# Optimization experiments

Measured on AMD Instinct MI355X. Metric: run time of the kernel, lower is better.

The kernel has to match this reference:

```python
import jax, jax.numpy as jnp
import numpy as np

BATCH, NUM_CENTERS, NUM_FEATURES = 8192, 2048, 512


def setup_inputs() -> dict:
    key = jax.random.key(0)
    k1, k2 = jax.random.split(key)
    inputs = jax.random.normal(k1, (BATCH, NUM_FEATURES), dtype=jnp.float32)
    centers = jax.random.normal(k2, (NUM_CENTERS, NUM_FEATURES), dtype=jnp.float32)
    sigmas = jnp.ones((NUM_CENTERS,), dtype=jnp.float32)
    return {"inputs": inputs, "centers": centers, "sigmas": sigmas}


def reference(inputs, centers, sigmas):
    # instead of materializing the [B, C, F] broadcast intermediate.
    x_sq = jnp.sum(inputs * inputs, axis=-1, keepdims=True)        # [B, 1]
    c_sq = jnp.sum(centers * centers, axis=-1)                     # [C]
    cross = jnp.einsum('bf,cf->bc', inputs, centers)               # [B, C]
    dists = x_sq + c_sq[None, :] - 2.0 * cross                     # [B, C]
    dists = jnp.maximum(dists, 0.0)  # guard tiny negatives from fp error
    return jnp.exp(-dists / (2.0 * sigmas * sigmas))               # [B, C]
```

## Files before the change

### kernel.cpp

```cpp
#include <hip/hip_runtime.h>
#include <hip/hip_bf16.h>
#include <stdint.h>


#define BATCH 8192
#define NCENT 2048
#define NFEAT 512

typedef float f32x4 __attribute__((ext_vector_type(4)));
typedef int   i32x8 __attribute__((ext_vector_type(8)));
typedef __bf16 bf16x8 __attribute__((ext_vector_type(8)));

union Frag8 {
    uint4 q[2];
    i32x8 v;
};
union FragAB {
    uint4 u;
    bf16x8 v;
};

static __device__ __forceinline__ unsigned int pack_bf16(float a, float b) {
    unsigned int ua = __builtin_bit_cast(unsigned int, a);
    unsigned int ub = __builtin_bit_cast(unsigned int, b);
    ua = (ua + 0x7fffu + ((ua >> 16) & 1u)) >> 16;
    ub = (ub + 0x7fffu + ((ub >> 16) & 1u)) >> 16;
    return ua | (ub << 16);
}

static __device__ __forceinline__ void llds16(const void* g, void* l) {
    __builtin_amdgcn_global_load_lds(
        (const __attribute__((address_space(1))) unsigned int*)g,
        (__attribute__((address_space(3))) unsigned int*)(uintptr_t)l,
        16, 0, 0);
}

__global__ __launch_bounds__(256) void convert_kernel(const float* __restrict__ X,
                                                      const float* __restrict__ Cn,
                                                      unsigned char* __restrict__ Xf8,
                                                      unsigned char* __restrict__ Cf8,
                                                      float* __restrict__ xsq,
                                                      float* __restrict__ csq) {
    const int bid  = blockIdx.x;
    const int lane = threadIdx.x & 63;
    const float* src;
    unsigned char* dst;
    float* nrm;
    int row;
    if (bid < BATCH / 4) {
        row = bid * 4 + (threadIdx.x >> 6);
        src = X; dst = Xf8; nrm = xsq;
    } else {
        row = (bid - BATCH / 4) * 4 + (threadIdx.x >> 6);
        src = Cn; dst = Cf8; nrm = csq;
    }
    const float4* p = (const float4*)(src + (size_t)row * NFEAT);
    float4 a = p[2 * lane];
    float4 b = p[2 * lane + 1];
    unsigned int lo = 0, hi = 0;
    lo = __builtin_amdgcn_cvt_pk_fp8_f32(a.x, a.y, lo, 0);
    lo = __builtin_amdgcn_cvt_pk_fp8_f32(a.z, a.w, lo, 1);
    hi = __builtin_amdgcn_cvt_pk_fp8_f32(b.x, b.y, hi, 0);
    hi = __builtin_amdgcn_cvt_pk_fp8_f32(b.z, b.w, hi, 1);
    ((uint2*)(dst + (size_t)row * NFEAT))[lane] = make_uint2(lo, hi);
    float s = a.x * a.x + a.y * a.y + a.z * a.z + a.w * a.w
            + b.x * b.x + b.y * b.y + b.z * b.z + b.w * b.w;
#pragma unroll
    for (int off = 32; off >= 1; off >>= 1) s += __shfl_down(s, off);
    if (lane == 0) nrm[row] = s;
}

__global__ __launch_bounds__(256) void rbf_gemm_fp8_kernel(
        const unsigned char* __restrict__ Xf8,
        const unsigned char* __restrict__ Cf8,
        const float* __restrict__ Sg,
        const float* __restrict__ xsq,
        const float* __restrict__ csq,
        float* __restrict__ out) {
    __shared__ unsigned char As[128 * 128];
    __shared__ unsigned char Bs[128 * 128];

    const int tid    = threadIdx.x;
    const int lane   = tid & 63;
    const int wave   = tid >> 6;
    const int wave_m = wave >> 1;
    const int wave_n = wave & 1;

    const int bid = blockIdx.x;
    const int xcd = bid & 7;
    const int j   = bid >> 3;
    const int bm0 = (xcd * 8 + (j >> 4)) * 128;
    const int bn0 = (j & 15) * 128;

    f32x4 acc[4][4];
#pragma unroll
    for (int i = 0; i < 4; ++i)
#pragma unroll
        for (int jj = 0; jj < 4; ++jj) acc[i][jj] = (f32x4){0.f, 0.f, 0.f, 0.f};

    const int fr   = lane & 15;
    const int quad = lane >> 4;

#pragma unroll
    for (int k0 = 0; k0 < NFEAT; k0 += 128) {
        __syncthreads();
#pragma unroll
        for (int i = 0; i < 4; ++i) {
            const int s   = (wave * 4 + i) * 64 + lane;
            const int row = s >> 3;
            const int c   = (s & 7) ^ (row & 7);
            llds16(Xf8 + (size_t)(bm0 + row) * NFEAT + k0 + c * 16,
                   As + (wave * 4 + i) * 1024);
            llds16(Cf8 + (size_t)(bn0 + row) * NFEAT + k0 + c * 16,
                   Bs + (wave * 4 + i) * 1024);
        }
        __syncthreads();

        Frag8 a[4], b[4];
#pragma unroll
        for (int mi = 0; mi < 4; ++mi) {
            const int row = wave_m * 64 + mi * 16 + fr;
            const unsigned char* base = As + row * 128;
            a[mi].q[0] = *(const uint4*)(base + ((quad * 2 + 0) ^ (row & 7)) * 16);
            a[mi].q[1] = *(const uint4*)(base + ((quad * 2 + 1) ^ (row & 7)) * 16);
        }
#pragma unroll
        for (int nj = 0; nj < 4; ++nj) {
            const int row = wave_n * 64 + nj * 16 + fr;
            const unsigned char* base = Bs + row * 128;
            b[nj].q[0] = *(const uint4*)(base + ((quad * 2 + 0) ^ (row & 7)) * 16);
            b[nj].q[1] = *(const uint4*)(base + ((quad * 2 + 1) ^ (row & 7)) * 16);
        }
#pragma unroll
        for (int mi = 0; mi < 4; ++mi)
#pragma unroll
            for (int nj = 0; nj < 4; ++nj)
                acc[mi][nj] = __builtin_amdgcn_mfma_scale_f32_16x16x128_f8f6f4(
                    a[mi].v, b[nj].v, acc[mi][nj],
                    0, 0,
                    0, 0x7F7F7F7F,
                    0, 0x7F7F7F7F);
    }

    const int col = lane & 15;
    const int rq  = lane >> 4;
#pragma unroll
    for (int nj = 0; nj < 4; ++nj) {
        const int n      = bn0 + wave_n * 64 + nj * 16 + col;
        const float csqn = csq[n];
        const float sg   = Sg[n];
        const float inv  = 0.5f / (sg * sg);
#pragma unroll
        for (int mi = 0; mi < 4; ++mi) {
            const int mbase = bm0 + wave_m * 64 + mi * 16 + rq * 4;
#pragma unroll
            for (int r = 0; r < 4; ++r) {
                const int m = mbase + r;
                float d = xsq[m] + csqn - 2.0f * acc[mi][nj][r];
                d = fmaxf(d, 0.0f);
                out[(size_t)m * NCENT + n] = __expf(-d * inv);
            }
        }
    }
}

__global__ __launch_bounds__(256) void sumsq_kernel(const float* __restrict__ src,
                                                    float* __restrict__ dst) {
    const int row  = blockIdx.x * 4 + (threadIdx.x >> 6);
    const int lane = threadIdx.x & 63;
    const float4* p = (const float4*)(src + (size_t)row * NFEAT);
    float4 a = p[lane];
    float4 b = p[lane + 64];
    float s = a.x * a.x + a.y * a.y + a.z * a.z + a.w * a.w
            + b.x * b.x + b.y * b.y + b.z * b.z + b.w * b.w;
#pragma unroll
    for (int off = 32; off >= 1; off >>= 1) s += __shfl_down(s, off);
    if (lane == 0) dst[row] = s;
}

__global__ __launch_bounds__(256) void rbf_fallback_kernel(const float* __restrict__ X,
                                                           const float* __restrict__ Cn,
                                                           const float* __restrict__ Sg,
                                                           const float* __restrict__ xsq,
                                                           const float* __restrict__ csq,
                                                           float* __restrict__ out) {
    __shared__ unsigned int As[128 * 16];
    __shared__ unsigned int Bs[128 * 16];

    const int tid    = threadIdx.x;
    const int lane   = tid & 63;
    const int wave   = tid >> 6;
    const int wave_m = wave >> 1;
    const int wave_n = wave & 1;
    const int bm0 = blockIdx.y * 128;
    const int bn0 = blockIdx.x * 128;

    f32x4 acc[4][4];
#pragma unroll
    for (int i = 0; i < 4; ++i)
#pragma unroll
        for (int j = 0; j < 4; ++j) acc[i][j] = (f32x4){0.f, 0.f, 0.f, 0.f};

    for (int k0 = 0; k0 < NFEAT; k0 += 32) {
        __syncthreads();
#pragma unroll
        for (int j = 0; j < 4; ++j) {
            const int s    = j * 256 + tid;
            const int row  = s >> 3;
            const int col4 = s & 7;
            {
                const float4 f = *(const float4*)(X + (size_t)(bm0 + row) * NFEAT + k0 + col4 * 4);
                *(uint2*)&As[row * 16 + col4 * 2] =
                    make_uint2(pack_bf16(f.x, f.y), pack_bf16(f.z, f.w));
            }
            {
                const float4 f = *(const float4*)(Cn + (size_t)(bn0 + row) * NFEAT + k0 + col4 * 4);
                *(uint2*)&Bs[row * 16 + col4 * 2] =
                    make_uint2(pack_bf16(f.x, f.y), pack_bf16(f.z, f.w));
            }
        }
        __syncthreads();

        const int fr   = lane & 15;
        const int quad = lane >> 4;
        FragAB a[4], b[4];
#pragma unroll
        for (int mi = 0; mi < 4; ++mi)
            a[mi].u = *(const uint4*)&As[(wave_m * 64 + mi * 16 + fr) * 16 + quad * 4];
#pragma unroll
        for (int nj = 0; nj < 4; ++nj)
            b[nj].u = *(const uint4*)&Bs[(wave_n * 64 + nj * 16 + fr) * 16 + quad * 4];
#pragma unroll
        for (int mi = 0; mi < 4; ++mi)
#pragma unroll
            for (int nj = 0; nj < 4; ++nj)
                acc[mi][nj] = __builtin_amdgcn_mfma_f32_16x16x32_bf16(
                    a[mi].v, b[nj].v, acc[mi][nj], 0, 0, 0);
    }

    const int col = lane & 15;
    const int rq  = lane >> 4;
#pragma unroll
    for (int nj = 0; nj < 4; ++nj) {
        const int n      = bn0 + wave_n * 64 + nj * 16 + col;
        const float csqn = csq[n];
        const float sg   = Sg[n];
        const float inv  = 0.5f / (sg * sg);
#pragma unroll
        for (int mi = 0; mi < 4; ++mi) {
            const int mbase = bm0 + wave_m * 64 + mi * 16 + rq * 4;
#pragma unroll
            for (int r = 0; r < 4; ++r) {
                const int m = mbase + r;
                float d = xsq[m] + csqn - 2.0f * acc[mi][nj][r];
                d = fmaxf(d, 0.0f);
                out[(size_t)m * NCENT + n] = __expf(-d * inv);
            }
        }
    }
}

extern "C" void kernel_launch(void* const* d_in, const int* in_sizes, int n_in,
                              void* d_out, int out_size, void* d_ws, size_t ws_size,
                              hipStream_t stream) {
    const float* X  = (const float*)d_in[0];
    const float* Cn = (const float*)d_in[1];
    const float* Sg = (const float*)d_in[2];
    float* out = (float*)d_out;

    const size_t xb = (size_t)BATCH * NFEAT;
    const size_t cb = (size_t)NCENT * NFEAT;
    const size_t need = xb + cb + (size_t)(BATCH + NCENT) * 4;

    if (ws_size >= need) {
        unsigned char* Xf8 = (unsigned char*)d_ws;
        unsigned char* Cf8 = Xf8 + xb;
        float* xsq = (float*)(Cf8 + cb);
        float* csq = xsq + BATCH;

        convert_kernel<<<(BATCH + NCENT) / 4, 256, 0, stream>>>(X, Cn, Xf8, Cf8, xsq, csq);
        rbf_gemm_fp8_kernel<<<1024, 256, 0, stream>>>(Xf8, Cf8, Sg, xsq, csq, out);
    } else {
        float* xsq = (float*)d_ws;
        float* csq = xsq + BATCH;
        sumsq_kernel<<<BATCH / 4, 256, 0, stream>>>(X, xsq);
        sumsq_kernel<<<NCENT / 4, 256, 0, stream>>>(Cn, csq);
        dim3 grid(NCENT / 128, BATCH / 128);
        rbf_fallback_kernel<<<grid, 256, 0, stream>>>(X, Cn, Sg, xsq, csq, out);
    }
}
```

Measured before the change: 99.79 us.

## Overlap next K-tile LDS load with MFMA and reorder convert kernel blocks

The GEMM loop now reads the current tile into registers, syncs, then issues the global-to-LDS load for the next K tile before running the MFMAs, so the memory latency can hide behind compute in the single LDS buffer. Launch bounds request three blocks per CU, which may cap registers. The convert kernel changes its load/store pattern to coalesced strided halves and permutes X row blocks across XCDs to match the GEMM's block mapping. The extra barrier per iteration and register pressure are the tradeoffs.

```diff
diff --git a/kernel.cpp b/kernel.cpp
--- a/kernel.cpp
+++ b/kernel.cpp
@@ -46,23 +46,26 @@
     const float* src;
     unsigned char* dst;
     float* nrm;
-    int row;
+    int rb;
     if (bid < BATCH / 4) {
-        row = bid * 4 + (threadIdx.x >> 6);
+        rb  = ((bid & 7) << 8) | (bid >> 3);
         src = X; dst = Xf8; nrm = xsq;
     } else {
-        row = (bid - BATCH / 4) * 4 + (threadIdx.x >> 6);
+        rb  = bid - BATCH / 4;
         src = Cn; dst = Cf8; nrm = csq;
     }
+    const int row = rb * 4 + (threadIdx.x >> 6);
     const float4* p = (const float4*)(src + (size_t)row * NFEAT);
-    float4 a = p[2 * lane];
-    float4 b = p[2 * lane + 1];
+    float4 a = p[lane];
+    float4 b = p[lane + 64];
     unsigned int lo = 0, hi = 0;
     lo = __builtin_amdgcn_cvt_pk_fp8_f32(a.x, a.y, lo, 0);
     lo = __builtin_amdgcn_cvt_pk_fp8_f32(a.z, a.w, lo, 1);
     hi = __builtin_amdgcn_cvt_pk_fp8_f32(b.x, b.y, hi, 0);
     hi = __builtin_amdgcn_cvt_pk_fp8_f32(b.z, b.w, hi, 1);
-    ((uint2*)(dst + (size_t)row * NFEAT))[lane] = make_uint2(lo, hi);
+    unsigned int* drow = (unsigned int*)(dst + (size_t)row * NFEAT);
+    drow[lane]      = lo;
+    drow[64 + lane] = hi;
     float s = a.x * a.x + a.y * a.y + a.z * a.z + a.w * a.w
             + b.x * b.x + b.y * b.y + b.z * b.z + b.w * b.w;
 #pragma unroll
@@ -70,7 +73,7 @@
     if (lane == 0) nrm[row] = s;
 }
 
-__global__ __launch_bounds__(256) void rbf_gemm_fp8_kernel(
+__global__ __launch_bounds__(256, 3) void rbf_gemm_fp8_kernel(
         const unsigned char* __restrict__ Xf8,
         const unsigned char* __restrict__ Cf8,
         const float* __restrict__ Sg,
@@ -101,19 +104,29 @@
     const int fr   = lane & 15;
     const int quad = lane >> 4;
 
-#pragma unroll
-    for (int k0 = 0; k0 < NFEAT; k0 += 128) {
-        __syncthreads();
-#pragma unroll
-        for (int i = 0; i < 4; ++i) {
-            const int s   = (wave * 4 + i) * 64 + lane;
-            const int row = s >> 3;
-            const int c   = (s & 7) ^ (row & 7);
-            llds16(Xf8 + (size_t)(bm0 + row) * NFEAT + k0 + c * 16,
-                   As + (wave * 4 + i) * 1024);
-            llds16(Cf8 + (size_t)(bn0 + row) * NFEAT + k0 + c * 16,
-                   Bs + (wave * 4 + i) * 1024);
-        }
+    const int s_row[4] = { ((wave * 4 + 0) * 64 + lane) >> 3,
+                           ((wave * 4 + 1) * 64 + lane) >> 3,
+                           ((wave * 4 + 2) * 64 + lane) >> 3,
+                           ((wave * 4 + 3) * 64 + lane) >> 3 };
+
+#define STAGE(K0)                                                              \
+    do {                                                                       \
+        _Pragma("unroll")                                                      \
+        for (int i = 0; i < 4; ++i) {                                          \
+            const int s   = (wave * 4 + i) * 64 + lane;                        \
+            const int row = s_row[i];                                          \
+            const int c   = (s & 7) ^ (row & 7);                               \
+            llds16(Xf8 + (size_t)(bm0 + row) * NFEAT + (K0) + c * 16,          \
+                   As + (wave * 4 + i) * 1024);                                \
+            llds16(Cf8 + (size_t)(bn0 + row) * NFEAT + (K0) + c * 16,          \
+                   Bs + (wave * 4 + i) * 1024);                                \
+        }                                                                      \
+    } while (0)
+
+    STAGE(0);
+
+#pragma unroll
+    for (int kt = 0; kt < 4; ++kt) {
         __syncthreads();
 
         Frag8 a[4], b[4];
@@ -131,6 +144,11 @@
             b[nj].q[0] = *(const uint4*)(base + ((quad * 2 + 0) ^ (row & 7)) * 16);
             b[nj].q[1] = *(const uint4*)(base + ((quad * 2 + 1) ^ (row & 7)) * 16);
         }
+
+        __syncthreads();
+
+        if (kt < 3) STAGE((kt + 1) * 128);
+
 #pragma unroll
         for (int mi = 0; mi < 4; ++mi)
 #pragma unroll
@@ -141,6 +159,7 @@
                     0, 0x7F7F7F7F,
                     0, 0x7F7F7F7F);
     }
+#undef STAGE
 
     const int col = lane & 15;
     const int rq  = lane >> 4;
```

Result: slower. 110.9 us (+11.1%).
